# Kernel tuning notes

Measured on AMD Instinct MI355X. Metric: run time of the kernel, lower is better.

## Reference

```python
import jax, jax.numpy as jnp
import numpy as np

N_ROWS = 200000
N_REFS = 2000000
X_DIM = 128
UNITS = 128


def setup_inputs() -> dict:
    key = jax.random.key(0)
    ks = jax.random.split(key, 8)
    X = jax.random.normal(ks[0], (N_ROWS, X_DIM), dtype=jnp.float32)
    ref_a = jax.random.randint(ks[1], (N_REFS,), 0, N_ROWS, dtype=jnp.int32)
    ref_b = jax.random.randint(ks[2], (N_REFS,), 0, N_ROWS, dtype=jnp.int32)
    backref = jax.random.randint(ks[3], (N_REFS,), 0, N_ROWS, dtype=jnp.int32)
    # Glorot-uniform-ish init for the three projections
    limit = np.sqrt(6.0 / (X_DIM + UNITS)).astype(np.float32)
    W_local = jax.random.uniform(ks[4], (X_DIM, UNITS), jnp.float32, -limit, limit)
    W_filter = jax.random.uniform(ks[5], (X_DIM, UNITS), jnp.float32, -limit, limit)
    W_neighbor = jax.random.uniform(ks[6], (X_DIM, UNITS), jnp.float32, -limit, limit)
    b = jnp.zeros((UNITS,), jnp.float32)
    b_neighbor = jnp.zeros((UNITS,), jnp.float32)
    return dict(X=X, ref_a=ref_a, ref_b=ref_b, backref=backref,
                W_local=W_local, W_filter=W_filter, W_neighbor=W_neighbor,
                b=b, b_neighbor=b_neighbor)


def reference(X, ref_a, ref_b, backref, W_local, W_filter, W_neighbor, b, b_neighbor):
    # Dense projections [N, units]
    XW_local = X @ W_local
    XW_filter = X @ W_filter
    XW_neighbor = X @ W_neighbor
    # wl2_convolution: gather pairs, combine (add + bias + inner relu), scatter-sum via backref
    msg = jax.nn.relu(XW_neighbor[ref_a] + XW_neighbor[ref_b] + b_neighbor)  # [M, units]
    X_conv = jax.ops.segment_sum(msg, backref, num_segments=X.shape[0])      # [N, units]
    X_agg = XW_local + XW_filter * X_conv + b
    return jax.nn.relu(X_agg)
```

## Files before the change

kernel.cpp:

```cpp
#include <hip/hip_runtime.h>


constexpr int DIM = 128;
constexpr int CAP = 40;

typedef _Float16 half_t;
typedef __attribute__((ext_vector_type(8))) _Float16 half8;
typedef __attribute__((ext_vector_type(4))) float f32x4;

__global__ __launch_bounds__(256) void transpose_w_k(
    const float* __restrict__ Wl, const float* __restrict__ Wf,
    const float* __restrict__ Wn, half_t* __restrict__ WlT,
    half_t* __restrict__ WfT, half_t* __restrict__ WnT) {
  __shared__ float t0[32][33], t1[32][33], t2[32][33];
  const int bx = (blockIdx.x & 3) * 32;
  const int by = (blockIdx.x >> 2) * 32;
  const int x = threadIdx.x & 31;
  const int y4 = (threadIdx.x >> 5) * 4;
#pragma unroll
  for (int i = 0; i < 4; ++i) {
    t0[y4 + i][x] = Wl[(by + y4 + i) * DIM + bx + x];
    t1[y4 + i][x] = Wf[(by + y4 + i) * DIM + bx + x];
    t2[y4 + i][x] = Wn[(by + y4 + i) * DIM + bx + x];
  }
  __syncthreads();
#pragma unroll
  for (int i = 0; i < 4; ++i) {
    WlT[(bx + y4 + i) * DIM + by + x] = (half_t)t0[x][y4 + i];
    WfT[(bx + y4 + i) * DIM + by + x] = (half_t)t1[x][y4 + i];
    WnT[(bx + y4 + i) * DIM + by + x] = (half_t)t2[x][y4 + i];
  }
}

__global__ __launch_bounds__(256) void fuseA_k(
    const float* __restrict__ X, const half_t* __restrict__ WnT,
    const float* __restrict__ bn, half_t* __restrict__ XWnh,
    const int* __restrict__ ra, const int* __restrict__ rb,
    const int* __restrict__ br, int* __restrict__ cnt,
    int2* __restrict__ slots, int Nrows, int E, int nbBlocks) {
  __shared__ half_t WT[DIM][136];
  const int g = blockIdx.x >> 1;
  const int tid = threadIdx.x;

  if (blockIdx.x & 1) {
    const int stride = nbBlocks * 256;
    for (int e = g * 256 + tid; e < E; e += stride) {
      const int row = br[e];
      const int pos = atomicAdd(&cnt[row], 1);
      if (pos < CAP) slots[(long)pos * Nrows + row] = make_int2(ra[e], rb[e]);
    }
    return;
  }

  for (int id = tid; id < 2048; id += 256) {
    const int u = id >> 4, c = (id & 15) * 8;
    *(half8*)(&WT[u][c]) = *(const half8*)(WnT + u * DIM + c);
  }
  __syncthreads();
  const int wave = tid >> 6, lane = tid & 63;
  const int ln = lane & 15, quad = lane >> 4;
  const long r0 = (long)g * 128 + wave * 32;
  f32x4 acc[2][8];
#pragma unroll
  for (int mt = 0; mt < 2; ++mt)
#pragma unroll
    for (int n = 0; n < 8; ++n) acc[mt][n] = (f32x4){0.f, 0.f, 0.f, 0.f};

  for (int kt = 0; kt < DIM; kt += 32) {
    half8 afr[2];
#pragma unroll
    for (int mt = 0; mt < 2; ++mt) {
      long row = r0 + mt * 16 + ln;
      if (row >= Nrows) row = Nrows - 1;
      const float* xp = X + row * DIM + kt + quad * 8;
      const float4 x0 = *(const float4*)xp;
      const float4 x1 = *(const float4*)(xp + 4);
      half8 a;
      a[0] = (half_t)x0.x; a[1] = (half_t)x0.y; a[2] = (half_t)x0.z; a[3] = (half_t)x0.w;
      a[4] = (half_t)x1.x; a[5] = (half_t)x1.y; a[6] = (half_t)x1.z; a[7] = (half_t)x1.w;
      afr[mt] = a;
    }
#pragma unroll
    for (int n = 0; n < 8; ++n) {
      const half8 b = *(const half8*)(&WT[n * 16 + ln][kt + quad * 8]);
      acc[0][n] = __builtin_amdgcn_mfma_f32_16x16x32_f16(afr[0], b, acc[0][n], 0, 0, 0);
      acc[1][n] = __builtin_amdgcn_mfma_f32_16x16x32_f16(afr[1], b, acc[1][n], 0, 0, 0);
    }
  }
#pragma unroll
  for (int n = 0; n < 8; ++n) {
    const int col = n * 16 + ln;
    const float bv = 0.5f * bn[col];
#pragma unroll
    for (int mt = 0; mt < 2; ++mt)
#pragma unroll
      for (int r = 0; r < 4; ++r) {
        const long row = r0 + mt * 16 + quad * 4 + r;
        if (row < Nrows) XWnh[row * DIM + col] = (half_t)(acc[mt][n][r] + bv);
      }
  }
}

__global__ __launch_bounds__(256) void gather_k(
    const half_t* __restrict__ XWnh, const int* __restrict__ cnt,
    const int2* __restrict__ slots, half_t* __restrict__ convh, int Nrows) {
  const int wave = threadIdx.x >> 6;
  const long row = (long)blockIdx.x * 4 + wave;
  if (row >= Nrows) return;
  const int lane = threadIdx.x & 63;
  const int sub = lane >> 4;
  const int sl = lane & 15;
  int c = cnt[row];
  if (c > CAP) c = CAP;
  float acc[8] = {0.f, 0.f, 0.f, 0.f, 0.f, 0.f, 0.f, 0.f};
  for (int p = sub; p < c; p += 4) {
    const int2 ab = slots[(long)p * Nrows + row];
    const half8 ha = *(const half8*)(XWnh + (long)ab.x * DIM + sl * 8);
    const half8 hb = *(const half8*)(XWnh + (long)ab.y * DIM + sl * 8);
#pragma unroll
    for (int j = 0; j < 8; ++j)
      acc[j] += fmaxf((float)ha[j] + (float)hb[j], 0.f);
  }
#pragma unroll
  for (int j = 0; j < 8; ++j) {
    acc[j] += __shfl_xor(acc[j], 16);
    acc[j] += __shfl_xor(acc[j], 32);
  }
  if (sub == 0) {
    half8 o;
#pragma unroll
    for (int j = 0; j < 8; ++j) o[j] = (half_t)acc[j];
    *(half8*)(convh + row * DIM + sl * 8) = o;
  }
}

__global__ __launch_bounds__(256, 4) void final_mfma_k(
    const float* __restrict__ X, const half_t* __restrict__ WlT,
    const half_t* __restrict__ WfT, const float* __restrict__ bias,
    const half_t* __restrict__ convh, float* __restrict__ out, int Nrows) {
  __shared__ half_t WTl[64][136];
  __shared__ half_t WTf[64][136];
  const int tid = threadIdx.x;
  const int wave = tid >> 6, lane = tid & 63;
  const int ln = lane & 15, quad = lane >> 4;
  const long r0 = (long)blockIdx.x * 128 + wave * 32;

  half8 afr[2][4];
#pragma unroll
  for (int mt = 0; mt < 2; ++mt) {
    long row = r0 + mt * 16 + ln;
    if (row >= Nrows) row = Nrows - 1;
    const float* xbase = X + row * DIM;
#pragma unroll
    for (int kt = 0; kt < 4; ++kt) {
      const float4 x0 = *(const float4*)(xbase + kt * 32 + quad * 8);
      const float4 x1 = *(const float4*)(xbase + kt * 32 + quad * 8 + 4);
      half8 a;
      a[0] = (half_t)x0.x; a[1] = (half_t)x0.y; a[2] = (half_t)x0.z; a[3] = (half_t)x0.w;
      a[4] = (half_t)x1.x; a[5] = (half_t)x1.y; a[6] = (half_t)x1.z; a[7] = (half_t)x1.w;
      afr[mt][kt] = a;
    }
  }

  for (int hf = 0; hf < 2; ++hf) {
    if (hf) __syncthreads();
    for (int id = tid; id < 1024; id += 256) {
      const int u = id >> 4, c = (id & 15) * 8;
      const size_t src = (size_t)(hf * 64 + u) * DIM + c;
      *(half8*)(&WTl[u][c]) = *(const half8*)(WlT + src);
      *(half8*)(&WTf[u][c]) = *(const half8*)(WfT + src);
    }
    __syncthreads();

    f32x4 accl[2][4], accf[2][4];
#pragma unroll
    for (int mt = 0; mt < 2; ++mt)
#pragma unroll
      for (int n = 0; n < 4; ++n) {
        accl[mt][n] = (f32x4){0.f, 0.f, 0.f, 0.f};
        accf[mt][n] = (f32x4){0.f, 0.f, 0.f, 0.f};
      }
#pragma unroll
    for (int kt = 0; kt < 4; ++kt)
#pragma unroll
      for (int n = 0; n < 4; ++n) {
        const half8 bl = *(const half8*)(&WTl[n * 16 + ln][kt * 32 + quad * 8]);
        const half8 bf = *(const half8*)(&WTf[n * 16 + ln][kt * 32 + quad * 8]);
        accl[0][n] = __builtin_amdgcn_mfma_f32_16x16x32_f16(afr[0][kt], bl, accl[0][n], 0, 0, 0);
        accl[1][n] = __builtin_amdgcn_mfma_f32_16x16x32_f16(afr[1][kt], bl, accl[1][n], 0, 0, 0);
        accf[0][n] = __builtin_amdgcn_mfma_f32_16x16x32_f16(afr[0][kt], bf, accf[0][n], 0, 0, 0);
        accf[1][n] = __builtin_amdgcn_mfma_f32_16x16x32_f16(afr[1][kt], bf, accf[1][n], 0, 0, 0);
      }

#pragma unroll
    for (int n = 0; n < 4; ++n) {
      const int col = hf * 64 + n * 16 + ln;
      const float bv = bias[col];
#pragma unroll
      for (int mt = 0; mt < 2; ++mt)
#pragma unroll
        for (int r = 0; r < 4; ++r) {
          const long orow = r0 + mt * 16 + quad * 4 + r;
          if (orow < Nrows) {
            const float cv = (float)convh[orow * DIM + col];
            out[orow * DIM + col] =
                fmaxf(accl[mt][n][r] + accf[mt][n][r] * cv + bv, 0.f);
          }
        }
    }
  }
}

extern "C" void kernel_launch(void* const* d_in, const int* in_sizes, int n_in,
                              void* d_out, int out_size, void* d_ws, size_t ws_size,
                              hipStream_t stream) {
  const float* X  = (const float*)d_in[0];
  const int* ra   = (const int*)d_in[1];
  const int* rb   = (const int*)d_in[2];
  const int* br   = (const int*)d_in[3];
  const float* Wl = (const float*)d_in[4];
  const float* Wf = (const float*)d_in[5];
  const float* Wn = (const float*)d_in[6];
  const float* b  = (const float*)d_in[7];
  const float* bn = (const float*)d_in[8];
  float* out = (float*)d_out;

  const int N = in_sizes[0] / DIM;
  const int E = in_sizes[1];

  half_t* XWnh = (half_t*)d_ws;
  half_t* convh = XWnh + (size_t)N * DIM;
  half_t* WlT = convh + (size_t)N * DIM;
  half_t* WfT = WlT + DIM * DIM;
  half_t* WnT = WfT + DIM * DIM;
  int* cnt = (int*)(WnT + DIM * DIM);
  int2* slots = (int2*)(cnt + ((N + 1) & ~1));

  hipMemsetAsync(cnt, 0, (size_t)N * sizeof(int), stream);
  transpose_w_k<<<16, 256, 0, stream>>>(Wl, Wf, Wn, WlT, WfT, WnT);

  const int nbBlocks = (N + 127) / 128;
  fuseA_k<<<2 * nbBlocks, 256, 0, stream>>>(X, WnT, bn, XWnh, ra, rb, br, cnt,
                                            slots, N, E, nbBlocks);
  gather_k<<<(N + 3) / 4, 256, 0, stream>>>(XWnh, cnt, slots, convh, N);
  final_mfma_k<<<nbBlocks, 256, 0, stream>>>(X, WlT, WfT, b, convh, out, N);
}
```

Baseline: 512.7 us.

## Store neighbor projection in FP8 and software-pipeline gather loads

The neighbor projection is now stored as FP8 (e4m3 via the packed convert builtin) instead of FP16, which halves the bytes read by the random-access gather. The gather loop is also restructured to prefetch slot indices two iterations ahead and row data one iteration ahead, so memory latency overlaps with the accumulation. The cost is a large loss of precision in the intermediate values, which may push the result past the tolerance. The FP8 stores are also single bytes per lane, which could be inefficient.

```diff
diff --git a/kernel.cpp b/kernel.cpp
--- a/kernel.cpp
+++ b/kernel.cpp
@@ -6,6 +6,7 @@
 
 typedef _Float16 half_t;
 typedef __attribute__((ext_vector_type(8))) _Float16 half8;
+typedef __attribute__((ext_vector_type(2))) float f32x2;
 typedef __attribute__((ext_vector_type(4))) float f32x4;
 
 __global__ __launch_bounds__(256) void transpose_w_k(
@@ -34,7 +35,7 @@
 
 __global__ __launch_bounds__(256) void fuseA_k(
     const float* __restrict__ X, const half_t* __restrict__ WnT,
-    const float* __restrict__ bn, half_t* __restrict__ XWnh,
+    const float* __restrict__ bn, unsigned char* __restrict__ XWnh8,
     const int* __restrict__ ra, const int* __restrict__ rb,
     const int* __restrict__ br, int* __restrict__ cnt,
     int2* __restrict__ slots, int Nrows, int E, int nbBlocks) {
@@ -96,13 +97,18 @@
 #pragma unroll
       for (int r = 0; r < 4; ++r) {
         const long row = r0 + mt * 16 + quad * 4 + r;
-        if (row < Nrows) XWnh[row * DIM + col] = (half_t)(acc[mt][n][r] + bv);
+        if (row < Nrows) {
+          const float v = acc[mt][n][r] + bv;
+          const unsigned int p =
+              __builtin_amdgcn_cvt_pk_fp8_f32(v, v, 0u, false);
+          XWnh8[row * DIM + col] = (unsigned char)(p & 0xffu);
+        }
       }
   }
 }
 
 __global__ __launch_bounds__(256) void gather_k(
-    const half_t* __restrict__ XWnh, const int* __restrict__ cnt,
+    const unsigned char* __restrict__ XWnh8, const int* __restrict__ cnt,
     const int2* __restrict__ slots, half_t* __restrict__ convh, int Nrows) {
   const int wave = threadIdx.x >> 6;
   const long row = (long)blockIdx.x * 4 + wave;
@@ -113,13 +119,40 @@
   int c = cnt[row];
   if (c > CAP) c = CAP;
   float acc[8] = {0.f, 0.f, 0.f, 0.f, 0.f, 0.f, 0.f, 0.f};
+
+  int2 abA = make_int2(0, 0), abB = make_int2(0, 0);
+  if (sub < c)     abA = slots[(long)sub * Nrows + row];
+  if (sub + 4 < c) abB = slots[(long)(sub + 4) * Nrows + row];
+  uint2 pAa = make_uint2(0u, 0u), pAb = make_uint2(0u, 0u);
+  if (sub < c) {
+    pAa = *(const uint2*)(XWnh8 + (long)abA.x * DIM + sl * 8);
+    pAb = *(const uint2*)(XWnh8 + (long)abA.y * DIM + sl * 8);
+  }
   for (int p = sub; p < c; p += 4) {
-    const int2 ab = slots[(long)p * Nrows + row];
-    const half8 ha = *(const half8*)(XWnh + (long)ab.x * DIM + sl * 8);
-    const half8 hb = *(const half8*)(XWnh + (long)ab.y * DIM + sl * 8);
-#pragma unroll
-    for (int j = 0; j < 8; ++j)
-      acc[j] += fmaxf((float)ha[j] + (float)hb[j], 0.f);
+    int2 abC = make_int2(0, 0);
+    if (p + 8 < c) abC = slots[(long)(p + 8) * Nrows + row];
+    uint2 pBa = make_uint2(0u, 0u), pBb = make_uint2(0u, 0u);
+    if (p + 4 < c) {
+      pBa = *(const uint2*)(XWnh8 + (long)abB.x * DIM + sl * 8);
+      pBb = *(const uint2*)(XWnh8 + (long)abB.y * DIM + sl * 8);
+    }
+    const f32x2 a01 = __builtin_amdgcn_cvt_pk_f32_fp8(pAa.x, false);
+    const f32x2 a23 = __builtin_amdgcn_cvt_pk_f32_fp8(pAa.x, true);
+    const f32x2 a45 = __builtin_amdgcn_cvt_pk_f32_fp8(pAa.y, false);
+    const f32x2 a67 = __builtin_amdgcn_cvt_pk_f32_fp8(pAa.y, true);
+    const f32x2 b01 = __builtin_amdgcn_cvt_pk_f32_fp8(pAb.x, false);
+    const f32x2 b23 = __builtin_amdgcn_cvt_pk_f32_fp8(pAb.x, true);
+    const f32x2 b45 = __builtin_amdgcn_cvt_pk_f32_fp8(pAb.y, false);
+    const f32x2 b67 = __builtin_amdgcn_cvt_pk_f32_fp8(pAb.y, true);
+    acc[0] += fmaxf(a01.x + b01.x, 0.f);
+    acc[1] += fmaxf(a01.y + b01.y, 0.f);
+    acc[2] += fmaxf(a23.x + b23.x, 0.f);
+    acc[3] += fmaxf(a23.y + b23.y, 0.f);
+    acc[4] += fmaxf(a45.x + b45.x, 0.f);
+    acc[5] += fmaxf(a45.y + b45.y, 0.f);
+    acc[6] += fmaxf(a67.x + b67.x, 0.f);
+    acc[7] += fmaxf(a67.y + b67.y, 0.f);
+    abA = abB; abB = abC; pAa = pBa; pAb = pBb;
   }
 #pragma unroll
   for (int j = 0; j < 8; ++j) {
@@ -228,8 +261,8 @@
   const int N = in_sizes[0] / DIM;
   const int E = in_sizes[1];
 
-  half_t* XWnh = (half_t*)d_ws;
-  half_t* convh = XWnh + (size_t)N * DIM;
+  unsigned char* XWnh8 = (unsigned char*)d_ws;
+  half_t* convh = (half_t*)(XWnh8 + (size_t)N * DIM);
   half_t* WlT = convh + (size_t)N * DIM;
   half_t* WfT = WlT + DIM * DIM;
   half_t* WnT = WfT + DIM * DIM;
@@ -240,8 +273,8 @@
   transpose_w_k<<<16, 256, 0, stream>>>(Wl, Wf, Wn, WlT, WfT, WnT);
 
   const int nbBlocks = (N + 127) / 128;
-  fuseA_k<<<2 * nbBlocks, 256, 0, stream>>>(X, WnT, bn, XWnh, ra, rb, br, cnt,
+  fuseA_k<<<2 * nbBlocks, 256, 0, stream>>>(X, WnT, bn, XWnh8, ra, rb, br, cnt,
                                             slots, N, E, nbBlocks);
-  gather_k<<<(N + 3) / 4, 256, 0, stream>>>(XWnh, cnt, slots, convh, N);
+  gather_k<<<(N + 3) / 4, 256, 0, stream>>>(XWnh8, cnt, slots, convh, N);
   final_mfma_k<<<nbBlocks, 256, 0, stream>>>(X, WlT, WfT, b, convh, out, N);
 }
```

New measurement: 470.2 us. 1.09x faster.
